# Optimization experiments

Hardware: AMD Instinct MI355X
Metric: run time of the kernel (lower is better)

The kernel has to match this reference:

```python
import jax, jax.numpy as jnp
import numpy as np

B, N, D = 16, 1024, 768
H = 12
HS = D // H
L = 2  # n_ffn_layers
EPS = 1e-6


def layernorm(x, scale, bias):
    mu = jnp.mean(x, axis=-1, keepdims=True)
    var = jnp.var(x, axis=-1, keepdims=True)
    return (x - mu) * jax.lax.rsqrt(var + EPS) * scale + bias


def log_cosh(x):
    # numerically stable log(cosh(x)) = |x| + log1p(exp(-2|x|)) - log(2)
    ax = jnp.abs(x)
    return ax + jnp.log1p(jnp.exp(-2.0 * ax)) - jnp.log(2.0)


def setup_inputs() -> dict:
    key = jax.random.key(0)
    ks = jax.random.split(key, 8)
    x = jax.random.normal(ks[0], (B, N, D), dtype=jnp.float32)
    # pre-attention LayerNorm params
    ln1_scale = jnp.ones((D,), jnp.float32)
    ln1_bias = jnp.zeros((D,), jnp.float32)
    # per-head value projections [H, D, HS] (Dense, no bias)
    Wv = jax.random.normal(ks[1], (H, D, HS), jnp.float32) / np.sqrt(D)
    # per-head circulant rows alpha_delta [H, N], truncated_normal(stddev=sqrt(1/N))
    alpha = jax.random.truncated_normal(ks[2], -2.0, 2.0, (H, N), jnp.float32) * np.sqrt(1.0 / N)
    # FFN: L layers of Dense(D) + LayerNorm + swish
    Wf = jax.random.normal(ks[3], (L, D, D), jnp.float32) / np.sqrt(D)
    bf = jnp.zeros((L, D), jnp.float32)
    lnf_scale = jnp.ones((L, D), jnp.float32)
    lnf_bias = jnp.zeros((L, D), jnp.float32)
    return {"x": x, "ln1_scale": ln1_scale, "ln1_bias": ln1_bias, "Wv": Wv,
            "alpha": alpha, "Wf": Wf, "bf": bf,
            "lnf_scale": lnf_scale, "lnf_bias": lnf_bias}


def reference(x, ln1_scale, ln1_bias, Wv, alpha, Wf, bf, lnf_scale, lnf_bias):
    b, n, d = x.shape
    h, hs = Wv.shape[0], Wv.shape[2]
    # --- multi-head positional (circulant) attention on LN(x) ---
    xn = layernorm(x, ln1_scale, ln1_bias)
    v = jnp.einsum('bnd,hdk->bhnk', xn, Wv)  # per-head values
    # circulant matrix C[h, i, j] = alpha[h, (i - j) mod n]  (scipy.linalg.circulant)
    idx = (jnp.arange(n)[:, None] - jnp.arange(n)[None, :]) % n  # [n, n]
    C = alpha[:, idx]                                            # [h, n, n]
    y = jnp.einsum('hij,bhjk->bhik', C, v)                       # [b, h, n, hs]
    y = jnp.transpose(y, (0, 2, 1, 3)).reshape(b, n, h * hs)     # concat heads
    x = x + y
    # --- FFN: [Dense(D) -> LayerNorm -> swish] x L ---
    z = x
    for l in range(Wf.shape[0]):
        z = jax.nn.swish(layernorm(z @ Wf[l] + bf[l], lnf_scale[l], lnf_bias[l]))
    return log_cosh(z + x)
```

## Files before the change

### kernel.cpp

```cpp
#include <hip/hip_runtime.h>
#include <cstdint>
#include <cstddef>


typedef __attribute__((ext_vector_type(8))) short bf16x8;
typedef __attribute__((ext_vector_type(4))) float f32x4;
typedef __attribute__((ext_vector_type(4))) unsigned short us4;

__device__ __forceinline__ unsigned short f2bf(float f) {
  unsigned int u = __builtin_bit_cast(unsigned int, f);
  u += 0x7FFFu + ((u >> 16) & 1u);
  return (unsigned short)(u >> 16);
}
__device__ __forceinline__ float bf2f(unsigned short u) {
  return __builtin_bit_cast(float, (unsigned int)u << 16);
}

__device__ __forceinline__ void g2l16(const void* g, void* l) {
  __builtin_amdgcn_global_load_lds(
      (const __attribute__((address_space(1))) unsigned int*)g,
      (__attribute__((address_space(3))) unsigned int*)l,
      16, 0, 0);
}

#define WAITB(n) asm volatile("s_waitcnt vmcnt(" #n ") lgkmcnt(0)\n\ts_barrier" ::: "memory")
#define BARX asm volatile("s_waitcnt lgkmcnt(0)\n\ts_barrier" ::: "memory")
#define BARV(n) asm volatile("s_waitcnt vmcnt(" #n ") lgkmcnt(0)\n\ts_barrier" ::: "memory")

__global__ __launch_bounds__(256) void pack_w2t(const float* __restrict__ Wv,
                                                unsigned short* __restrict__ W2t) {
  int o = blockIdx.x * 256 + threadIdx.x;
  int np = o / 768, d = o - np * 768;
  int h = np >> 6, k = np & 63;
  W2t[o] = f2bf(Wv[h * 49152 + d * 64 + k]);
}

__global__ __launch_bounds__(256) void pack_wft(const float* __restrict__ Wf,
                                                unsigned short* __restrict__ Wft) {
  int o = blockIdx.x * 256 + threadIdx.x;
  int l = o / 589824, rem = o - l * 589824;
  int np = rem / 768, d = rem - np * 768;
  Wft[o] = f2bf(Wf[l * 589824 + d * 768 + np]);
}

__device__ __forceinline__ void wave_reduce2(float& s, float& s2) {
#pragma unroll
  for (int off = 32; off > 0; off >>= 1) {
    s += __shfl_down(s, off);
    s2 += __shfl_down(s2, off);
  }
  s = __shfl(s, 0);
  s2 = __shfl(s2, 0);
}

__global__ __launch_bounds__(256) void ln1_kernel(const float* __restrict__ x,
                                                  const float* __restrict__ sc,
                                                  const float* __restrict__ bi,
                                                  unsigned short* __restrict__ out) {
  int row = blockIdx.x * 4 + (threadIdx.x >> 6);
  int lane = threadIdx.x & 63;
  size_t base = (size_t)row * 768;
  float4 v[3];
#pragma unroll
  for (int j = 0; j < 3; ++j) v[j] = *(const float4*)(x + base + lane * 4 + j * 256);
  float s = 0.f, s2 = 0.f;
#pragma unroll
  for (int j = 0; j < 3; ++j) {
    s += v[j].x + v[j].y + v[j].z + v[j].w;
    s2 += v[j].x * v[j].x + v[j].y * v[j].y + v[j].z * v[j].z + v[j].w * v[j].w;
  }
  wave_reduce2(s, s2);
  float mu = s * (1.0f / 768.0f);
  float var = s2 * (1.0f / 768.0f) - mu * mu;
  float r = rsqrtf(var + 1e-6f);
#pragma unroll
  for (int j = 0; j < 3; ++j) {
    int d = lane * 4 + j * 256;
    float4 scv = *(const float4*)(sc + d);
    float4 biv = *(const float4*)(bi + d);
    us4 o;
    o[0] = f2bf((v[j].x - mu) * r * scv.x + biv.x);
    o[1] = f2bf((v[j].y - mu) * r * scv.y + biv.y);
    o[2] = f2bf((v[j].z - mu) * r * scv.z + biv.z);
    o[3] = f2bf((v[j].w - mu) * r * scv.w + biv.w);
    *(us4*)(out + base + d) = o;
  }
}

__global__ __launch_bounds__(256) void lnswish_kernel(const unsigned short* __restrict__ g,
                                                      const float* __restrict__ sc,
                                                      const float* __restrict__ bi,
                                                      unsigned short* __restrict__ out) {
  int row = blockIdx.x * 4 + (threadIdx.x >> 6);
  int lane = threadIdx.x & 63;
  size_t base = (size_t)row * 768;
  float v[3][4];
#pragma unroll
  for (int j = 0; j < 3; ++j) {
    us4 gv = *(const us4*)(g + base + lane * 4 + j * 256);
#pragma unroll
    for (int q = 0; q < 4; ++q) v[j][q] = bf2f(gv[q]);
  }
  float s = 0.f, s2 = 0.f;
#pragma unroll
  for (int j = 0; j < 3; ++j)
#pragma unroll
    for (int q = 0; q < 4; ++q) { s += v[j][q]; s2 += v[j][q] * v[j][q]; }
  wave_reduce2(s, s2);
  float mu = s * (1.0f / 768.0f);
  float var = s2 * (1.0f / 768.0f) - mu * mu;
  float r = rsqrtf(var + 1e-6f);
#pragma unroll
  for (int j = 0; j < 3; ++j) {
    int d = lane * 4 + j * 256;
    float4 scv = *(const float4*)(sc + d);
    float4 biv = *(const float4*)(bi + d);
    const float* scp = &scv.x;
    const float* bip = &biv.x;
    us4 o;
#pragma unroll
    for (int q = 0; q < 4; ++q) {
      float z = (v[j][q] - mu) * r * scp[q] + bip[q];
      o[q] = f2bf(z / (1.0f + __expf(-z)));
    }
    *(us4*)(out + base + d) = o;
  }
}

__global__ __launch_bounds__(256) void final_kernel(const unsigned short* __restrict__ g,
                                                    const float* __restrict__ sc,
                                                    const float* __restrict__ bi,
                                                    const unsigned short* __restrict__ x2,
                                                    float* __restrict__ out) {
  int row = blockIdx.x * 4 + (threadIdx.x >> 6);
  int lane = threadIdx.x & 63;
  size_t base = (size_t)row * 768;
  float v[3][4];
#pragma unroll
  for (int j = 0; j < 3; ++j) {
    us4 gv = *(const us4*)(g + base + lane * 4 + j * 256);
#pragma unroll
    for (int q = 0; q < 4; ++q) v[j][q] = bf2f(gv[q]);
  }
  float s = 0.f, s2 = 0.f;
#pragma unroll
  for (int j = 0; j < 3; ++j)
#pragma unroll
    for (int q = 0; q < 4; ++q) { s += v[j][q]; s2 += v[j][q] * v[j][q]; }
  wave_reduce2(s, s2);
  float mu = s * (1.0f / 768.0f);
  float var = s2 * (1.0f / 768.0f) - mu * mu;
  float r = rsqrtf(var + 1e-6f);
#pragma unroll
  for (int j = 0; j < 3; ++j) {
    int d = lane * 4 + j * 256;
    float4 scv = *(const float4*)(sc + d);
    float4 biv = *(const float4*)(bi + d);
    us4 xv = *(const us4*)(x2 + base + d);
    const float* scp = &scv.x;
    const float* bip = &biv.x;
    float4 o;
    float* op = &o.x;
#pragma unroll
    for (int q = 0; q < 4; ++q) {
      float z = (v[j][q] - mu) * r * scp[q] + bip[q];
      float sw = z / (1.0f + __expf(-z));
      float t = sw + bf2f(xv[q]);
      float ax = fabsf(t);
      op[q] = ax + __logf(1.0f + __expf(-2.0f * ax)) - 0.69314718055994531f;
    }
    *(float4*)(out + base + d) = o;
  }
}

template <int K>
__device__ __forceinline__ void gemm256(const unsigned short* __restrict__ A,
                                        const unsigned short* __restrict__ Bt,
                                        int m0, int n0, unsigned short* lds,
                                        f32x4 acc[8][4]) {
  const int tid = threadIdx.x;
  const int lane = tid & 63;
  const int wid = tid >> 6;
  const int wm = (wid >> 2) << 6;
  const int wn = (wid & 3) << 5;
  const int fm = lane & 15, fq = lane >> 4;
  const int srow = tid >> 3;
  const int sslot = (tid & 7) ^ (srow & 7);
  const size_t abase = (size_t)(m0 + srow) * K + (sslot << 3);
  const size_t bbase = (size_t)(n0 + srow) * K + (sslot << 3);

  bf16x8 aq[4][2], bq[4][2];

#define STG_A(kt, bb, c)                                                     \
  g2l16(A + abase + (size_t)((c) << 6) * K + ((kt) << 6),                    \
        lds + ((bb) << 15) + ((c) << 12) + (tid << 3))
#define STG_B(kt, bb, c)                                                     \
  g2l16(Bt + bbase + (size_t)((c) << 6) * K + ((kt) << 6),                   \
        lds + ((bb) << 15) + 16384 + ((c) << 12) + (tid << 3))
#define LDA(bb, mh)                                                          \
  _Pragma("unroll") for (int mt = 0; mt < 4; ++mt) {                         \
    const unsigned short* p =                                                \
        lds + ((bb) << 15) + (wm + ((mh) << 7) + (mt << 4) + fm) * 64;       \
    _Pragma("unroll") for (int kk = 0; kk < 2; ++kk)                         \
      aq[mt][kk] = *(const bf16x8*)(p + ((((kk << 2) + fq) ^ (fm & 7)) << 3)); \
  }
#define LDB(bb, nh)                                                          \
  _Pragma("unroll") for (int nt = 0; nt < 2; ++nt) {                         \
    const unsigned short* p = lds + ((bb) << 15) + 16384 +                   \
                              (wn + ((nh) << 7) + (nt << 4) + fm) * 64;      \
    _Pragma("unroll") for (int kk = 0; kk < 2; ++kk)                         \
      bq[((nh) << 1) + nt][kk] =                                             \
          *(const bf16x8*)(p + ((((kk << 2) + fq) ^ (fm & 7)) << 3));        \
  }
#define MMX(mh, nh)                                                          \
  {                                                                          \
    __builtin_amdgcn_s_setprio(1);                                           \
    _Pragma("unroll") for (int mt = 0; mt < 4; ++mt)                         \
    _Pragma("unroll") for (int nt = 0; nt < 2; ++nt)                         \
    _Pragma("unroll") for (int kk = 0; kk < 2; ++kk)                         \
      acc[((mh) << 2) + mt][((nh) << 1) + nt] =                              \
          __builtin_amdgcn_mfma_f32_16x16x32_bf16(                           \
              aq[mt][kk], bq[((nh) << 1) + nt][kk],                          \
              acc[((mh) << 2) + mt][((nh) << 1) + nt], 0, 0, 0);             \
    __builtin_amdgcn_s_setprio(0);                                           \
  }

  constexpr int NT = K >> 6;
  STG_A(0, 0, 0); STG_A(0, 0, 1); STG_A(0, 0, 2); STG_A(0, 0, 3);
  STG_B(0, 0, 0); STG_B(0, 0, 1); STG_B(0, 0, 2); STG_B(0, 0, 3);
  STG_A(1, 1, 0); STG_A(1, 1, 1);
  STG_B(1, 1, 0); STG_B(1, 1, 1);
  BARV(4);

  for (int t = 0; t < (NT >> 1) - 1; ++t) {
    const int k1 = 2 * t + 1, k2 = 2 * t + 2, k3 = 2 * t + 3;
    LDA(0, 0); LDB(0, 0);
    STG_A(k1, 1, 2); STG_A(k1, 1, 3);
    MMX(0, 0); BARX;
    LDB(0, 1);
    STG_B(k1, 1, 2); STG_B(k1, 1, 3);
    MMX(0, 1); BARX;
    LDA(0, 1);
    STG_A(k2, 0, 0); STG_A(k2, 0, 1);
    MMX(1, 0); BARX;
    STG_B(k2, 0, 0); STG_B(k2, 0, 1);
    MMX(1, 1); BARV(4);
    LDA(1, 0); LDB(1, 0);
    STG_A(k2, 0, 2); STG_A(k2, 0, 3);
    MMX(0, 0); BARX;
    LDB(1, 1);
    STG_B(k2, 0, 2); STG_B(k2, 0, 3);
    MMX(0, 1); BARX;
    LDA(1, 1);
    STG_A(k3, 1, 0); STG_A(k3, 1, 1);
    MMX(1, 0); BARX;
    STG_B(k3, 1, 0); STG_B(k3, 1, 1);
    MMX(1, 1); BARV(4);
  }
  {
    const int k1 = NT - 1;
    LDA(0, 0); LDB(0, 0);
    STG_A(k1, 1, 2); STG_A(k1, 1, 3);
    MMX(0, 0); BARX;
    LDB(0, 1);
    STG_B(k1, 1, 2); STG_B(k1, 1, 3);
    MMX(0, 1); BARX;
    LDA(0, 1);
    MMX(1, 0); BARX;
    MMX(1, 1);
    BARV(0);
    LDA(1, 0); LDB(1, 0);
    MMX(0, 0); BARX;
    LDB(1, 1);
    MMX(0, 1); BARX;
    LDA(1, 1);
    MMX(1, 0); BARX;
    MMX(1, 1);
  }
#undef STG_A
#undef STG_B
#undef LDA
#undef LDB
#undef MMX
}

__device__ __forceinline__ void decode256(int bid, int& m0, int& n0) {
  int wg = (bid & 7) * 24 + (bid >> 3);
  int mi = wg / 3, ni = wg - mi * 3;
  m0 = mi << 8;
  n0 = ni << 8;
}

__global__ __launch_bounds__(512, 2) void gemm1_256(const unsigned short* __restrict__ A,
                                                    const unsigned short* __restrict__ W2t,
                                                    unsigned short* __restrict__ Vt) {
  extern __shared__ unsigned short lds[];
  f32x4 acc[8][4] = {};
  int m0, n0;
  decode256(blockIdx.x, m0, n0);
  gemm256<768>(A, W2t, m0, n0, lds, acc);
  const int lane = threadIdx.x & 63, wid = threadIdx.x >> 6;
  const int wm = (wid >> 2) << 6, wn = (wid & 3) << 5;
  const int fm = lane & 15, fq = lane >> 4;
#pragma unroll
  for (int ai = 0; ai < 8; ++ai) {
    int rowb = m0 + wm + ((ai >> 2) << 7) + ((ai & 3) << 4) + (fq << 2);
    int b = rowb >> 10, n = rowb & 1023;
#pragma unroll
    for (int nj = 0; nj < 4; ++nj) {
      int col = n0 + wn + ((nj >> 1) << 7) + ((nj & 1) << 4) + fm;
      int h = col >> 6, ck = col & 63;
      size_t off = ((size_t)h << 20) + (size_t)((b << 6) + ck) * 1024 + n;
      us4 v;
#pragma unroll
      for (int r = 0; r < 4; ++r) v[r] = f2bf(acc[ai][nj][r]);
      *(us4*)(Vt + off) = v;
    }
  }
}

__global__ __launch_bounds__(512, 2) void gemmf_256(const unsigned short* __restrict__ A,
                                                    const unsigned short* __restrict__ Bt,
                                                    const float* __restrict__ bias,
                                                    unsigned short* __restrict__ g) {
  extern __shared__ unsigned short lds[];
  f32x4 acc[8][4] = {};
  int m0, n0;
  decode256(blockIdx.x, m0, n0);
  gemm256<768>(A, Bt, m0, n0, lds, acc);
  const int lane = threadIdx.x & 63, wid = threadIdx.x >> 6;
  const int wm = (wid >> 2) << 6, wn = (wid & 3) << 5;
  const int fm = lane & 15, fq = lane >> 4;
#pragma unroll
  for (int ai = 0; ai < 8; ++ai) {
    int rowb = m0 + wm + ((ai >> 2) << 7) + ((ai & 3) << 4) + (fq << 2);
#pragma unroll
    for (int nj = 0; nj < 4; ++nj) {
      int col = n0 + wn + ((nj >> 1) << 7) + ((nj & 1) << 4) + fm;
      float bc = bias[col];
#pragma unroll
      for (int r = 0; r < 4; ++r)
        g[(size_t)(rowb + r) * 768 + col] = f2bf(acc[ai][nj][r] + bc);
    }
  }
}

__global__ __launch_bounds__(256, 3) void circ_kernel(const float* __restrict__ alpha,
                                                      const unsigned short* __restrict__ Vt,
                                                      const float* __restrict__ xin,
                                                      unsigned short* __restrict__ x2bf) {
  __shared__ unsigned short sAc[8 * 1168];
  __shared__ unsigned short sB[4 * 4096];
  f32x4 acc[4][4] = {};
  int f = blockIdx.x;
  int xcd = f & 7, s = f >> 3;
  int h = s >> 3, t = s & 7;
  int mr = xcd >> 1, nr = xcd & 1;
  int m0 = ((mr << 1) + (t >> 2)) << 7;
  int n0 = ((nr << 2) + (t & 3)) << 7;

  const int tid = threadIdx.x;
  const int wave = tid >> 6, lane = tid & 63;
  const int wm = (wave >> 1) << 6, wn = (wave & 1) << 6;
  const int fm = lane & 15, fq = lane >> 4;

  const float* ah = alpha + (h << 10);
#pragma unroll
  for (int c = 0; c < 8; ++c)
    for (int u = tid; u < 1160; u += 256)
      sAc[c * 1168 + u] = f2bf(ah[(m0 - 897 - u - c) & 1023]);
  asm volatile("s_waitcnt vmcnt(0)" ::: "memory");

  const unsigned short* Bt = Vt + ((size_t)h << 20);
  const int r0 = tid >> 2, r1 = r0 + 64;
  const int cg = tid & 3;
  const int cs0 = (cg ^ ((r0 >> 1) & 3)) << 3;
  const int cs1 = (cg ^ ((r1 >> 1) & 3)) << 3;
  const int ld0 = r0 * 32 + (cg << 3);
  const int ld1 = r1 * 32 + (cg << 3);

#define STAGEB(k0v, buf)                                                      \
  {                                                                           \
    unsigned short* dB = sB + (buf) * 4096;                                   \
    g2l16(Bt + (size_t)(n0 + r0) * 1024 + (k0v) + cs0, dB + ld0);             \
    g2l16(Bt + (size_t)(n0 + r1) * 1024 + (k0v) + cs1, dB + ld1);             \
  }
#define CCOMP(it)                                                             \
  {                                                                           \
    const unsigned short* pB = sB + ((it) & 3) * 4096;                        \
    int k0v = (it) << 5;                                                      \
    bf16x8 aq[4], bq[4];                                                      \
    _Pragma("unroll") for (int t_ = 0; t_ < 4; ++t_) {                        \
      int rl = wm + (t_ << 4) + fm;                                           \
      int d = k0v + (fq << 3) + 127 - rl;                                     \
      int c = d & 7;                                                          \
      aq[t_] = *(const bf16x8*)(sAc + c * 1168 + (d - c));                    \
      int rb = wn + (t_ << 4) + fm;                                           \
      bq[t_] = *(const bf16x8*)(pB + (rb << 5) + ((fq ^ ((rb >> 1) & 3)) << 3)); \
    }                                                                         \
    _Pragma("unroll") for (int mt = 0; mt < 4; ++mt)                          \
    _Pragma("unroll") for (int nt = 0; nt < 4; ++nt)                          \
      acc[mt][nt] = __builtin_amdgcn_mfma_f32_16x16x32_bf16(aq[mt], bq[nt],   \
                                                            acc[mt][nt], 0, 0, 0); \
  }

  STAGEB(0, 0);
  STAGEB(32, 1);
  STAGEB(64, 2);
  for (int it = 0; it < 30; ++it) {
    WAITB(4);
    if (it < 29) STAGEB((it + 3) << 5, (it + 3) & 3);
    CCOMP(it);
  }
  WAITB(2);
  CCOMP(30);
  WAITB(0);
  CCOMP(31);
#undef STAGEB

#pragma unroll
  for (int mt = 0; mt < 4; ++mt) {
    int ib = m0 + wm + (mt << 4) + (fq << 2);
#pragma unroll
    for (int nt = 0; nt < 4; ++nt) {
      int c = n0 + wn + (nt << 4) + fm;
      int b = c >> 6, k = c & 63;
      size_t off = ((size_t)(b << 10) + ib) * 768 + (h << 6) + k;
#pragma unroll
      for (int r = 0; r < 4; ++r) {
        float val = acc[mt][nt][r] + xin[off + (size_t)r * 768];
        x2bf[off + (size_t)r * 768] = f2bf(val);
      }
    }
  }
}

extern "C" void kernel_launch(void* const* d_in, const int* in_sizes, int n_in,
                              void* d_out, int out_size, void* d_ws, size_t ws_size,
                              hipStream_t stream) {
  const float* x = (const float*)d_in[0];
  const float* ln1_s = (const float*)d_in[1];
  const float* ln1_b = (const float*)d_in[2];
  const float* Wv = (const float*)d_in[3];
  const float* alpha = (const float*)d_in[4];
  const float* Wf = (const float*)d_in[5];
  const float* bf = (const float*)d_in[6];
  const float* lnf_s = (const float*)d_in[7];
  const float* lnf_b = (const float*)d_in[8];
  float* out = (float*)d_out;

  char* ws = (char*)d_ws;
  unsigned short* slotA = (unsigned short*)ws;
  unsigned short* Vt = (unsigned short*)(ws + 25165824);
  unsigned short* gbf = Vt;
  unsigned short* slotX = (unsigned short*)(ws + 50331648);
  unsigned short* W2t = (unsigned short*)(ws + 75497472);
  unsigned short* Wft = (unsigned short*)(ws + 76677120);

  hipFuncSetAttribute((const void*)gemm1_256,
                      hipFuncAttributeMaxDynamicSharedMemorySize, 131072);
  hipFuncSetAttribute((const void*)gemmf_256,
                      hipFuncAttributeMaxDynamicSharedMemorySize, 131072);

  pack_w2t<<<2304, 256, 0, stream>>>(Wv, W2t);
  pack_wft<<<4608, 256, 0, stream>>>(Wf, Wft);

  ln1_kernel<<<4096, 256, 0, stream>>>(x, ln1_s, ln1_b, slotA);
  gemm1_256<<<192, 512, 131072, stream>>>(slotA, W2t, Vt);
  circ_kernel<<<768, 256, 0, stream>>>(alpha, Vt, x, slotX);
  gemmf_256<<<192, 512, 131072, stream>>>(slotX, Wft, bf, gbf);
  lnswish_kernel<<<4096, 256, 0, stream>>>(gbf, lnf_s, lnf_b, slotA);
  gemmf_256<<<192, 512, 131072, stream>>>(slotA, Wft + 589824, bf + 768, gbf);
  final_kernel<<<4096, 256, 0, stream>>>(gbf, lnf_s + 768, lnf_b + 768, slotX, out);
}
```

Measured before the change: 278.4 us.

## Retile circulant matmul to 256x256 tiles with 8-wave ping-pong pipeline; merge pack kernels

Replaces the 128x128-tile circulant kernel (768 blocks, 256 threads) with a 256x256-tile version using 512 threads, 64-wide K steps, double-buffered B staging interleaved with MFMA quarters and setprio hints, and a larger shifted-alpha table in dynamic LDS. This raises reuse per loaded tile and overlaps global-to-LDS loads with compute. The two weight-packing kernels are also merged into one launch to save launch overhead. The risks are fewer blocks (192 on a 256-CU device), higher register pressure from the 8x4 accumulators, and more barriers per K step.

```diff
diff --git a/kernel.cpp b/kernel.cpp
--- a/kernel.cpp
+++ b/kernel.cpp
@@ -23,24 +23,25 @@
       16, 0, 0);
 }
 
-#define WAITB(n) asm volatile("s_waitcnt vmcnt(" #n ") lgkmcnt(0)\n\ts_barrier" ::: "memory")
 #define BARX asm volatile("s_waitcnt lgkmcnt(0)\n\ts_barrier" ::: "memory")
 #define BARV(n) asm volatile("s_waitcnt vmcnt(" #n ") lgkmcnt(0)\n\ts_barrier" ::: "memory")
 
-__global__ __launch_bounds__(256) void pack_w2t(const float* __restrict__ Wv,
-                                                unsigned short* __restrict__ W2t) {
-  int o = blockIdx.x * 256 + threadIdx.x;
-  int np = o / 768, d = o - np * 768;
-  int h = np >> 6, k = np & 63;
-  W2t[o] = f2bf(Wv[h * 49152 + d * 64 + k]);
-}
-
-__global__ __launch_bounds__(256) void pack_wft(const float* __restrict__ Wf,
+__global__ __launch_bounds__(256) void pack_all(const float* __restrict__ Wv,
+                                                const float* __restrict__ Wf,
+                                                unsigned short* __restrict__ W2t,
                                                 unsigned short* __restrict__ Wft) {
-  int o = blockIdx.x * 256 + threadIdx.x;
-  int l = o / 589824, rem = o - l * 589824;
-  int np = rem / 768, d = rem - np * 768;
-  Wft[o] = f2bf(Wf[l * 589824 + d * 768 + np]);
+  int bid = blockIdx.x;
+  if (bid < 2304) {
+    int o = bid * 256 + threadIdx.x;
+    int np = o / 768, d = o - np * 768;
+    int h = np >> 6, k = np & 63;
+    W2t[o] = f2bf(Wv[h * 49152 + d * 64 + k]);
+  } else {
+    int o = (bid - 2304) * 256 + threadIdx.x;
+    int l = o / 589824, rem = o - l * 589824;
+    int np = rem / 768, d = rem - np * 768;
+    Wft[o] = f2bf(Wf[l * 589824 + d * 768 + np]);
+  }
 }
 
 __device__ __forceinline__ void wave_reduce2(float& s, float& s2) {
@@ -345,90 +346,131 @@
   }
 }
 
-__global__ __launch_bounds__(256, 3) void circ_kernel(const float* __restrict__ alpha,
-                                                      const unsigned short* __restrict__ Vt,
-                                                      const float* __restrict__ xin,
-                                                      unsigned short* __restrict__ x2bf) {
-  __shared__ unsigned short sAc[8 * 1168];
-  __shared__ unsigned short sB[4 * 4096];
-  f32x4 acc[4][4] = {};
-  int f = blockIdx.x;
-  int xcd = f & 7, s = f >> 3;
-  int h = s >> 3, t = s & 7;
-  int mr = xcd >> 1, nr = xcd & 1;
-  int m0 = ((mr << 1) + (t >> 2)) << 7;
-  int n0 = ((nr << 2) + (t & 3)) << 7;
+__global__ __launch_bounds__(512, 2) void circ256_kernel(const float* __restrict__ alpha,
+                                                         const unsigned short* __restrict__ Vt,
+                                                         const float* __restrict__ xin,
+                                                         unsigned short* __restrict__ x2bf) {
+  extern __shared__ unsigned short lds[];
+  unsigned short* sAc = lds;
+  unsigned short* sB = lds + 10304;
+  f32x4 acc[8][4] = {};
+
+  int wg = (blockIdx.x & 7) * 24 + (blockIdx.x >> 3);
+  int h = wg >> 4, tt = wg & 15;
+  int m0 = (tt >> 2) << 8, n0 = (tt & 3) << 8;
 
   const int tid = threadIdx.x;
-  const int wave = tid >> 6, lane = tid & 63;
-  const int wm = (wave >> 1) << 6, wn = (wave & 1) << 6;
+  const int lane = tid & 63, wid = tid >> 6;
+  const int wm = (wid >> 2) << 6, wn = (wid & 3) << 5;
   const int fm = lane & 15, fq = lane >> 4;
+  const int srow = tid >> 3;
+  const int sslot = (tid & 7) ^ (srow & 7);
 
   const float* ah = alpha + (h << 10);
 #pragma unroll
   for (int c = 0; c < 8; ++c)
-    for (int u = tid; u < 1160; u += 256)
-      sAc[c * 1168 + u] = f2bf(ah[(m0 - 897 - u - c) & 1023]);
-  asm volatile("s_waitcnt vmcnt(0)" ::: "memory");
+    for (int u = tid; u < 1280; u += 512)
+      sAc[c * 1288 + u] = f2bf(ah[(m0 - 769 - u - c) & 1023]);
 
   const unsigned short* Bt = Vt + ((size_t)h << 20);
-  const int r0 = tid >> 2, r1 = r0 + 64;
-  const int cg = tid & 3;
-  const int cs0 = (cg ^ ((r0 >> 1) & 3)) << 3;
-  const int cs1 = (cg ^ ((r1 >> 1) & 3)) << 3;
-  const int ld0 = r0 * 32 + (cg << 3);
-  const int ld1 = r1 * 32 + (cg << 3);
-
-#define STAGEB(k0v, buf)                                                      \
-  {                                                                           \
-    unsigned short* dB = sB + (buf) * 4096;                                   \
-    g2l16(Bt + (size_t)(n0 + r0) * 1024 + (k0v) + cs0, dB + ld0);             \
-    g2l16(Bt + (size_t)(n0 + r1) * 1024 + (k0v) + cs1, dB + ld1);             \
-  }
-#define CCOMP(it)                                                             \
-  {                                                                           \
-    const unsigned short* pB = sB + ((it) & 3) * 4096;                        \
-    int k0v = (it) << 5;                                                      \
-    bf16x8 aq[4], bq[4];                                                      \
-    _Pragma("unroll") for (int t_ = 0; t_ < 4; ++t_) {                        \
-      int rl = wm + (t_ << 4) + fm;                                           \
-      int d = k0v + (fq << 3) + 127 - rl;                                     \
-      int c = d & 7;                                                          \
-      aq[t_] = *(const bf16x8*)(sAc + c * 1168 + (d - c));                    \
-      int rb = wn + (t_ << 4) + fm;                                           \
-      bq[t_] = *(const bf16x8*)(pB + (rb << 5) + ((fq ^ ((rb >> 1) & 3)) << 3)); \
-    }                                                                         \
-    _Pragma("unroll") for (int mt = 0; mt < 4; ++mt)                          \
-    _Pragma("unroll") for (int nt = 0; nt < 4; ++nt)                          \
-      acc[mt][nt] = __builtin_amdgcn_mfma_f32_16x16x32_bf16(aq[mt], bq[nt],   \
-                                                            acc[mt][nt], 0, 0, 0); \
-  }
-
-  STAGEB(0, 0);
-  STAGEB(32, 1);
-  STAGEB(64, 2);
-  for (int it = 0; it < 30; ++it) {
-    WAITB(4);
-    if (it < 29) STAGEB((it + 3) << 5, (it + 3) & 3);
-    CCOMP(it);
-  }
-  WAITB(2);
-  CCOMP(30);
-  WAITB(0);
-  CCOMP(31);
-#undef STAGEB
-
-#pragma unroll
-  for (int mt = 0; mt < 4; ++mt) {
-    int ib = m0 + wm + (mt << 4) + (fq << 2);
-#pragma unroll
-    for (int nt = 0; nt < 4; ++nt) {
-      int c = n0 + wn + (nt << 4) + fm;
-      int b = c >> 6, k = c & 63;
-      size_t off = ((size_t)(b << 10) + ib) * 768 + (h << 6) + k;
+  const size_t bbase = (size_t)(n0 + srow) * 1024 + (sslot << 3);
+
+  bf16x8 aq[4][2], bq[4][2];
+
+#define CSTG(kt, bb, c)                                                      \
+  g2l16(Bt + bbase + (size_t)((c) << 6) * 1024 + ((kt) << 6),                \
+        sB + ((bb) << 14) + ((c) << 12) + (tid << 3))
+#define CLDA(kt, mh)                                                         \
+  _Pragma("unroll") for (int mt = 0; mt < 4; ++mt)                           \
+  _Pragma("unroll") for (int kk = 0; kk < 2; ++kk) {                         \
+    int d_ = ((kt) << 6) + (kk << 5) + (fq << 3) + 255 -                     \
+             (wm + ((mh) << 7) + (mt << 4) + fm);                            \
+    int c_ = d_ & 7;                                                         \
+    aq[mt][kk] = *(const bf16x8*)(sAc + c_ * 1288 + (d_ - c_));              \
+  }
+#define CLDB(bb, nh)                                                         \
+  _Pragma("unroll") for (int nt = 0; nt < 2; ++nt) {                         \
+    const unsigned short* p =                                                \
+        sB + ((bb) << 14) + (wn + ((nh) << 7) + (nt << 4) + fm) * 64;        \
+    _Pragma("unroll") for (int kk = 0; kk < 2; ++kk)                         \
+      bq[((nh) << 1) + nt][kk] =                                             \
+          *(const bf16x8*)(p + ((((kk << 2) + fq) ^ (fm & 7)) << 3));        \
+  }
+#define CMMX(mh, nh)                                                         \
+  {                                                                          \
+    __builtin_amdgcn_s_setprio(1);                                           \
+    _Pragma("unroll") for (int mt = 0; mt < 4; ++mt)                         \
+    _Pragma("unroll") for (int nt = 0; nt < 2; ++nt)                         \
+    _Pragma("unroll") for (int kk = 0; kk < 2; ++kk)                         \
+      acc[((mh) << 2) + mt][((nh) << 1) + nt] =                              \
+          __builtin_amdgcn_mfma_f32_16x16x32_bf16(                           \
+              aq[mt][kk], bq[((nh) << 1) + nt][kk],                          \
+              acc[((mh) << 2) + mt][((nh) << 1) + nt], 0, 0, 0);             \
+    __builtin_amdgcn_s_setprio(0);                                           \
+  }
+
+  CSTG(0, 0, 0); CSTG(0, 0, 1); CSTG(0, 0, 2); CSTG(0, 0, 3);
+  CSTG(1, 1, 0); CSTG(1, 1, 1);
+  BARV(2);
+
+  for (int it = 0; it < 7; ++it) {
+    const int k0 = 2 * it, k1 = 2 * it + 1, k2 = 2 * it + 2, k3 = 2 * it + 3;
+    CLDA(k0, 0); CLDB(0, 0);
+    CSTG(k1, 1, 2);
+    CMMX(0, 0); BARX;
+    CLDB(0, 1);
+    CSTG(k1, 1, 3);
+    CMMX(0, 1); BARX;
+    CLDA(k0, 1);
+    CSTG(k2, 0, 0);
+    CMMX(1, 0); BARX;
+    CSTG(k2, 0, 1);
+    CMMX(1, 1); BARV(2);
+    CLDA(k1, 0); CLDB(1, 0);
+    CSTG(k2, 0, 2);
+    CMMX(0, 0); BARX;
+    CLDB(1, 1);
+    CSTG(k2, 0, 3);
+    CMMX(0, 1); BARX;
+    CLDA(k1, 1);
+    CSTG(k3, 1, 0);
+    CMMX(1, 0); BARX;
+    CSTG(k3, 1, 1);
+    CMMX(1, 1); BARV(2);
+  }
+  CLDA(14, 0); CLDB(0, 0);
+  CSTG(15, 1, 2);
+  CMMX(0, 0); BARX;
+  CLDB(0, 1);
+  CSTG(15, 1, 3);
+  CMMX(0, 1); BARX;
+  CLDA(14, 1);
+  CMMX(1, 0); BARX;
+  CMMX(1, 1);
+  BARV(0);
+  CLDA(15, 0); CLDB(1, 0);
+  CMMX(0, 0); BARX;
+  CLDB(1, 1);
+  CMMX(0, 1); BARX;
+  CLDA(15, 1);
+  CMMX(1, 0); BARX;
+  CMMX(1, 1);
+#undef CSTG
+#undef CLDA
+#undef CLDB
+#undef CMMX
+
+#pragma unroll
+  for (int ai = 0; ai < 8; ++ai) {
+    int i = m0 + wm + ((ai >> 2) << 7) + ((ai & 3) << 4) + (fq << 2);
+#pragma unroll
+    for (int nj = 0; nj < 4; ++nj) {
+      int col = n0 + wn + ((nj >> 1) << 7) + ((nj & 1) << 4) + fm;
+      int b = col >> 6, k = col & 63;
+      size_t off = ((size_t)(b << 10) + i) * 768 + (h << 6) + k;
 #pragma unroll
       for (int r = 0; r < 4; ++r) {
-        float val = acc[mt][nt][r] + xin[off + (size_t)r * 768];
+        float val = acc[ai][nj][r] + xin[off + (size_t)r * 768];
         x2bf[off + (size_t)r * 768] = f2bf(val);
       }
     }
@@ -461,13 +503,14 @@
                       hipFuncAttributeMaxDynamicSharedMemorySize, 131072);
   hipFuncSetAttribute((const void*)gemmf_256,
                       hipFuncAttributeMaxDynamicSharedMemorySize, 131072);
-
-  pack_w2t<<<2304, 256, 0, stream>>>(Wv, W2t);
-  pack_wft<<<4608, 256, 0, stream>>>(Wf, Wft);
+  hipFuncSetAttribute((const void*)circ256_kernel,
+                      hipFuncAttributeMaxDynamicSharedMemorySize, 86144);
+
+  pack_all<<<6912, 256, 0, stream>>>(Wv, Wf, W2t, Wft);
 
   ln1_kernel<<<4096, 256, 0, stream>>>(x, ln1_s, ln1_b, slotA);
   gemm1_256<<<192, 512, 131072, stream>>>(slotA, W2t, Vt);
-  circ_kernel<<<768, 256, 0, stream>>>(alpha, Vt, x, slotX);
+  circ256_kernel<<<192, 512, 86144, stream>>>(alpha, Vt, x, slotX);
   gemmf_256<<<192, 512, 131072, stream>>>(slotX, Wft, bf, gbf);
   lnswish_kernel<<<4096, 256, 0, stream>>>(gbf, lnf_s, lnf_b, slotA);
   gemmf_256<<<192, 512, 131072, stream>>>(slotA, Wft + 589824, bf + 768, gbf);
```

New measurement: 270.3 us. 1.03x faster.
